# Optimization experiments

Hardware: AMD Instinct MI355X
Metric: run time of the kernel (lower is better)

Reference implementation:

```python
import jax, jax.numpy as jnp
import numpy as np

H = 8  # num_heads

def setup_inputs() -> dict:
    key = jax.random.key(0)
    ks = jax.random.split(key, 10)
    B, N, D, E = 1, 4096, 256, 65536
    s = 0.02
    return {
        "x": jax.random.normal(ks[0], (B, N, D), jnp.float32),
        "edge_index": jax.random.randint(ks[1], (2, E), 0, N, jnp.int32),
        "edge_attr": jax.random.normal(ks[2], (E, 3), jnp.float32),
        "Wq": jax.random.normal(ks[3], (D, D), jnp.float32) * s,
        "bq": jnp.zeros((D,), jnp.float32),
        "Wk": jax.random.normal(ks[4], (D, D), jnp.float32) * s,
        "bk": jnp.zeros((D,), jnp.float32),
        "Wv": jax.random.normal(ks[5], (D, D), jnp.float32) * s,
        "bv": jnp.zeros((D,), jnp.float32),
        "Wo": jax.random.normal(ks[6], (D, D), jnp.float32) * s,
        "bo": jnp.zeros((D,), jnp.float32),
        "We": jax.random.normal(ks[7], (3, H), jnp.float32) * s,
        "be": jnp.zeros((H,), jnp.float32),
    }

def reference(x, edge_index, edge_attr, Wq, bq, Wk, bk, Wv, bv, Wo, bo, We, be):
    B, N, D = x.shape
    hd = D // H
    q = (x @ Wq + bq).reshape(B, N, H, hd)
    k = (x @ Wk + bk).reshape(B, N, H, hd)
    v = (x @ Wv + bv).reshape(B, N, H, hd)
    # scores: [B, H, N, N]
    scores = jnp.einsum("bihd,bjhd->bhij", q, k) / jnp.sqrt(jnp.asarray(hd, x.dtype))
    # edge bias: torch scatter_ writes a row-constant value into column edge_tgt
    # for every query row (edge_src unused in the original). Equivalent to a
    # per-head column bias [H, N], broadcast over batch and query rows.
    eb = edge_attr @ We + be            # [E, H]
    edge_tgt = edge_index[1]
    col_bias = jnp.zeros((H, N), x.dtype).at[:, edge_tgt].set(eb.T)  # [H, N]
    scores = scores + col_bias[None, :, None, :]
    attn = jax.nn.softmax(scores, axis=-1)
    out = jnp.einsum("bhij,bjhd->bihd", attn, v).reshape(B, N, D)
    return out @ Wo + bo
```

## Files before the change

### kernel.cpp

```cpp
#include <hip/hip_runtime.h>
#include <hip/hip_bf16.h>
#include <math.h>

#define NUM_H 8
#define HD 32
#define DD 256
#define NSPLIT 2
#define KVBLK 64

typedef __attribute__((ext_vector_type(8))) short bf16x8;
typedef __attribute__((ext_vector_type(4))) float f32x4;

__device__ __forceinline__ unsigned short f2b(float f) {
  unsigned u = __builtin_bit_cast(unsigned, f);
  u += 0x7FFFu + ((u >> 16) & 1u);
  return (unsigned short)(u >> 16);
}

__device__ __forceinline__ unsigned pack2(float a, float b) {
  float2 t; t.x = a; t.y = b;
  __hip_bfloat162 r = __float22bfloat162_rn(t);
  unsigned u;
  __builtin_memcpy(&u, &r, sizeof(u));
  return u;
}

#define LOG2E 1.4426950408889634f


__global__ void sel_scatter_kernel(const int* __restrict__ tgt, int* __restrict__ sel, int E) {
  int e = blockIdx.x * 256 + threadIdx.x;
  if (e < E) atomicMax(&sel[tgt[e]], e);
}

__global__ void cvt_all(const float* __restrict__ W0, const float* __restrict__ W1,
                        const float* __restrict__ W2, const float* __restrict__ W3,
                        unsigned short* __restrict__ T0, unsigned short* __restrict__ T1,
                        unsigned short* __restrict__ T2, unsigned short* __restrict__ T3,
                        const float* __restrict__ x, unsigned short* __restrict__ xf,
                        int* __restrict__ sel, int N) {
  const int z = blockIdx.z;
  const int tid = threadIdx.x;
  if (z == 5) {
    const int b = blockIdx.x * 8 + blockIdx.y;
    if (b < (N + 255) / 256) {
      int t = b * 256 + tid;
      if (t < N) sel[t] = -1;
    }
    return;
  }
  if (z == 4) {
    const int b = blockIdx.x * 8 + blockIdx.y;
    const int ntiles = N / 16;
    for (int tt = 0; tt < ntiles / 64; ++tt) {
      const int t4 = b * (ntiles / 64) + tt;
#pragma unroll
      for (int gi = 0; gi < 2; ++gi) {
        const int g = tid + gi * 256;
        const int lr = g >> 5, kk = (g >> 2) & 7, lg = g & 3;
        const float* src = x + ((size_t)t4 * 16 + lr) * DD + kk * 32 + lg * 8;
        const float4 a = *reinterpret_cast<const float4*>(src);
        const float4 c = *reinterpret_cast<const float4*>(src + 4);
        uint4 o;
        o.x = pack2(a.x, a.y); o.y = pack2(a.z, a.w);
        o.z = pack2(c.x, c.y); o.w = pack2(c.z, c.w);
        *reinterpret_cast<uint4*>(xf + (size_t)t4 * 4096 + kk * 512 + lg * 128 + lr * 8) = o;
      }
    }
    return;
  }
  __shared__ float t[32][33];
  const float* W = (z == 0) ? W0 : (z == 1) ? W1 : (z == 2) ? W2 : W3;
  unsigned short* WF = (z == 0) ? T0 : (z == 1) ? T1 : (z == 2) ? T2 : T3;
  const int bx = blockIdx.x, by = blockIdx.y;
  const int lx = tid & 31, ly = tid >> 5;
#pragma unroll
  for (int r = 0; r < 32; r += 8)
    t[r + ly][lx] = W[(size_t)(bx * 32 + r + ly) * DD + by * 32 + lx];
  __syncthreads();
  if (tid < 128) {
    const int ct = tid & 31, lg = tid >> 5;
    bf16x8 val;
#pragma unroll
    for (int e = 0; e < 8; ++e)
      val[e] = (short)f2b(t[lg * 8 + e][ct]);
    const int off = (by * 8 + bx) * 1024 + (ct >> 4) * 512 + lg * 128 + (ct & 15) * 8;
    *reinterpret_cast<bf16x8*>(WF + off) = val;
  }
}

__global__ __launch_bounds__(256) void proj_qkv(const unsigned short* __restrict__ Xf,
                                                const unsigned short* __restrict__ WTq,
                                                const unsigned short* __restrict__ WTk,
                                                const unsigned short* __restrict__ WTv,
                                                const float* __restrict__ bq,
                                                const float* __restrict__ bk,
                                                const float* __restrict__ bv,
                                                unsigned short* __restrict__ qfrag,
                                                unsigned short* __restrict__ kfrag,
                                                unsigned short* __restrict__ vfrag,
                                                const int* __restrict__ sel,
                                                const float* __restrict__ ea,
                                                const float* __restrict__ We,
                                                const float* __restrict__ be,
                                                float* __restrict__ biasg, int N) {
  const int z = blockIdx.z;
  const int tid = threadIdx.x;
  if (z == 3) {
    const int b = blockIdx.x * 8 + blockIdx.y;
    if (b >= (N + 255) / 256) return;
    const int t = b * 256 + tid;
    if (t >= N) return;
    int e = sel[t];
    bool has = (e >= 0);
    float a0 = 0.f, a1 = 0.f, a2 = 0.f;
    if (has) {
      a0 = ea[3 * (size_t)e];
      a1 = ea[3 * (size_t)e + 1];
      a2 = ea[3 * (size_t)e + 2];
    }
#pragma unroll
    for (int h = 0; h < NUM_H; ++h) {
      float v = has ? (a0 * We[h] + a1 * We[NUM_H + h] + a2 * We[2 * NUM_H + h] + be[h]) : 0.f;
      biasg[(size_t)h * N + t] = v * LOG2E;
    }
    return;
  }
  const unsigned short* WT = (z == 0) ? WTq : (z == 1) ? WTk : WTv;
  const float* bias = (z == 0) ? bq : (z == 1) ? bk : bv;
  const int w = tid >> 6, l = tid & 63;
  const int lr = l & 15, lg = l >> 4;
  const int nt = blockIdx.x * 4 + w;
  const int n0 = nt * 16;
  const int cb = blockIdx.y;
  const int c0 = cb * 32;
  const int NT = N / 16;
  const f32x4 zero4 = {0.f, 0.f, 0.f, 0.f};
  f32x4 acc0 = zero4, acc1 = zero4;
  const unsigned short* ap = Xf + (size_t)nt * 4096 + lg * 128 + lr * 8;
  const unsigned short* bp = WT + (size_t)cb * 8192 + lg * 128 + lr * 8;
  if (z < 2) {
#pragma unroll
    for (int kk = 0; kk < 8; ++kk) {
      bf16x8 a  = *reinterpret_cast<const bf16x8*>(ap + kk * 512);
      bf16x8 b0 = *reinterpret_cast<const bf16x8*>(bp + kk * 1024);
      bf16x8 b1 = *reinterpret_cast<const bf16x8*>(bp + kk * 1024 + 512);
      acc0 = __builtin_amdgcn_mfma_f32_16x16x32_bf16(b0, a, acc0, 0, 0, 0);
      acc1 = __builtin_amdgcn_mfma_f32_16x16x32_bf16(b1, a, acc1, 0, 0, 0);
    }
    const f32x4 bv0 = *reinterpret_cast<const f32x4*>(bias + c0 + lg * 4);
    const f32x4 bv1 = *reinterpret_cast<const f32x4*>(bias + c0 + 16 + lg * 4);
    unsigned short* QK = z ? kfrag : qfrag;
    size_t base;
    int rowoff;
    if (z == 1) {
      const int j = ((nt & 3) << 4) + lr;
      const int pos = ((j >> 5) * 2 + ((j >> 2) & 1)) * 16 + (((j & 31) >> 3) << 2) + (j & 3);
      const int t16p = ((nt >> 2) << 2) + (pos >> 4);
      base = ((size_t)cb * NT + t16p) * 512;
      rowoff = (pos & 15) * 8;
    } else {
      base = ((size_t)cb * NT + nt) * 512;
      rowoff = lr * 8;
    }
    const int kf0 = (lg >> 1) * 128, ke = (lg & 1) * 4;
    uint2 o0, o1;
    o0.x = pack2(acc0[0] + bv0[0], acc0[1] + bv0[1]);
    o0.y = pack2(acc0[2] + bv0[2], acc0[3] + bv0[3]);
    o1.x = pack2(acc1[0] + bv1[0], acc1[1] + bv1[1]);
    o1.y = pack2(acc1[2] + bv1[2], acc1[3] + bv1[3]);
    *reinterpret_cast<uint2*>(QK + base + kf0 + rowoff + ke) = o0;
    *reinterpret_cast<uint2*>(QK + base + 256 + kf0 + rowoff + ke) = o1;
  } else {
#pragma unroll
    for (int kk = 0; kk < 8; ++kk) {
      bf16x8 a  = *reinterpret_cast<const bf16x8*>(ap + kk * 512);
      bf16x8 b0 = *reinterpret_cast<const bf16x8*>(bp + kk * 1024);
      bf16x8 b1 = *reinterpret_cast<const bf16x8*>(bp + kk * 1024 + 512);
      acc0 = __builtin_amdgcn_mfma_f32_16x16x32_bf16(a, b0, acc0, 0, 0, 0);
      acc1 = __builtin_amdgcn_mfma_f32_16x16x32_bf16(a, b1, acc1, 0, 0, 0);
    }
    const float bc0 = bias[c0 + lr], bc1 = bias[c0 + 16 + lr];
    const int lgf = ((n0 & 16) >> 3) + (lg >> 1);
    const int ke = (lg & 1) * 4;
    const size_t vbase = ((size_t)cb * (N / 32) + (n0 >> 5)) * 1024;
    uint2 o0, o1;
    o0.x = pack2(acc0[0] + bc0, acc0[1] + bc0);
    o0.y = pack2(acc0[2] + bc0, acc0[3] + bc0);
    o1.x = pack2(acc1[0] + bc1, acc1[1] + bc1);
    o1.y = pack2(acc1[2] + bc1, acc1[3] + bc1);
    *reinterpret_cast<uint2*>(vfrag + vbase + lgf * 128 + lr * 8 + ke) = o0;
    *reinterpret_cast<uint2*>(vfrag + vbase + 512 + lgf * 128 + lr * 8 + ke) = o1;
  }
}

__global__ __launch_bounds__(256) void proj_out(const unsigned short* __restrict__ Obf,
                                                const unsigned short* __restrict__ WT,
                                                const float* __restrict__ bias,
                                                float* __restrict__ Y, int N) {
  const int w = threadIdx.x >> 6, l = threadIdx.x & 63;
  const int lr = l & 15, lg = l >> 4;
  const int nt = blockIdx.x * 4 + w;
  const int n0 = nt * 16;
  const int cb = blockIdx.y;
  const int c0 = cb * 32;
  const f32x4 zero4 = {0.f, 0.f, 0.f, 0.f};
  f32x4 acc0 = zero4, acc1 = zero4;
  const unsigned short* ap = Obf + (size_t)nt * 4096 + lg * 128 + lr * 8;
  const unsigned short* bp = WT + (size_t)cb * 8192 + lg * 128 + lr * 8;
#pragma unroll
  for (int kk = 0; kk < 8; ++kk) {
    bf16x8 a  = *reinterpret_cast<const bf16x8*>(ap + kk * 512);
    bf16x8 b0 = *reinterpret_cast<const bf16x8*>(bp + kk * 1024);
    bf16x8 b1 = *reinterpret_cast<const bf16x8*>(bp + kk * 1024 + 512);
    acc0 = __builtin_amdgcn_mfma_f32_16x16x32_bf16(a, b0, acc0, 0, 0, 0);
    acc1 = __builtin_amdgcn_mfma_f32_16x16x32_bf16(a, b1, acc1, 0, 0, 0);
  }
  const float bc0 = bias[c0 + lr], bc1 = bias[c0 + 16 + lr];
#pragma unroll
  for (int r = 0; r < 4; ++r) {
    Y[(size_t)(n0 + lg * 4 + r) * DD + c0 + lr]      = acc0[r] + bc0;
    Y[(size_t)(n0 + lg * 4 + r) * DD + c0 + 16 + lr] = acc1[r] + bc1;
  }
}

__device__ __forceinline__ void attn_tile(const bf16x8 qf, const bf16x8* kf, const bf16x8* vf,
                                          const float* __restrict__ Bs, int tbase, int lg,
                                          float scl2, float& lsum, f32x4& oacc0, f32x4& oacc1) {
  const f32x4 zero4 = {0.f, 0.f, 0.f, 0.f};
  f32x4 sc[4];
  __builtin_amdgcn_s_setprio(1);
#pragma unroll
  for (int jf = 0; jf < 4; ++jf)
    sc[jf] = __builtin_amdgcn_mfma_f32_16x16x32_bf16(kf[jf], qf, zero4, 0, 0, 0);
  __builtin_amdgcn_s_setprio(0);

  float rsum = 0.f;
  unsigned pk[8];
#pragma unroll
  for (int jf = 0; jf < 4; ++jf) {
    const f32x4 b4 = *reinterpret_cast<const f32x4*>(
        &Bs[tbase + (jf >> 1) * 32 + lg * 8 + (jf & 1) * 4]);
    float e0 = __builtin_amdgcn_exp2f(sc[jf][0] * scl2 + b4[0]);
    float e1 = __builtin_amdgcn_exp2f(sc[jf][1] * scl2 + b4[1]);
    float e2 = __builtin_amdgcn_exp2f(sc[jf][2] * scl2 + b4[2]);
    float e3 = __builtin_amdgcn_exp2f(sc[jf][3] * scl2 + b4[3]);
    rsum += (e0 + e1) + (e2 + e3);
    pk[jf * 2]     = pack2(e0, e1);
    pk[jf * 2 + 1] = pack2(e2, e3);
  }
  rsum += __shfl_xor(rsum, 16);
  rsum += __shfl_xor(rsum, 32);
  lsum += rsum;

  bf16x8 pfA, pfB;
  __builtin_memcpy(&pfA, &pk[0], 16);
  __builtin_memcpy(&pfB, &pk[4], 16);
  __builtin_amdgcn_s_setprio(1);
  oacc0 = __builtin_amdgcn_mfma_f32_16x16x32_bf16(pfA, vf[0], oacc0, 0, 0, 0);
  oacc1 = __builtin_amdgcn_mfma_f32_16x16x32_bf16(pfA, vf[1], oacc1, 0, 0, 0);
  oacc0 = __builtin_amdgcn_mfma_f32_16x16x32_bf16(pfB, vf[2], oacc0, 0, 0, 0);
  oacc1 = __builtin_amdgcn_mfma_f32_16x16x32_bf16(pfB, vf[3], oacc1, 0, 0, 0);
  __builtin_amdgcn_s_setprio(0);
}

__global__ __launch_bounds__(256, 4) void attn_mfma(const unsigned short* __restrict__ qfrag,
                                                    const unsigned short* __restrict__ kfrag,
                                                    const unsigned short* __restrict__ vfrag,
                                                    const float* __restrict__ biasg,
                                                    float* __restrict__ Opart,
                                                    float* __restrict__ lpart, int N) {
  __shared__ float Bs[2048];
  const int tid = threadIdx.x;
  const int w = tid >> 6, l = tid & 63;
  const int lr = l & 15, lg = l >> 4;
  const int bid = blockIdx.x;
  const int h = bid & 7;
  const int rem = bid >> 3;
  const int qblk = rem & 63;
  const int s = rem >> 6;
  const int q0 = qblk * 64 + w * 16;
  const int NT = N / 16;
  const int jlo = s * (N / NSPLIT);
  const float scl2 = 0.17677669529663687f * LOG2E;

  const bf16x8 qf = *reinterpret_cast<const bf16x8*>(
      qfrag + ((size_t)h * NT + (q0 >> 4)) * 512 + l * 8);

#pragma unroll
  for (int i = 0; i < 2; ++i)
    *reinterpret_cast<float4*>(&Bs[tid * 4 + i * 1024]) =
        *reinterpret_cast<const float4*>(biasg + (size_t)h * N + jlo + tid * 4 + i * 1024);
  __syncthreads();

  const unsigned short* kb_ = kfrag + ((size_t)h * NT + (jlo >> 4)) * 512 + l * 8;
  const unsigned short* vb_ = vfrag + ((size_t)h * (N / 32) + (jlo >> 5)) * 1024 + l * 8;

  float lsum = 0.f;
  const f32x4 zero4 = {0.f, 0.f, 0.f, 0.f};
  f32x4 oacc0 = zero4, oacc1 = zero4;

#define LOADK(dst, t)                                                               \
  {                                                                                 \
    _Pragma("unroll") for (int jf = 0; jf < 4; ++jf)                                \
        dst[jf] = *reinterpret_cast<const bf16x8*>(kb_ + ((t) * 4 + jf) * 512);     \
  }
#define LOADV(dst, t)                                                               \
  {                                                                                 \
    _Pragma("unroll") for (int cd = 0; cd < 4; ++cd)                                \
        dst[cd] = *reinterpret_cast<const bf16x8*>(vb_ + ((t) * 2 + (cd >> 1)) * 1024 \
                                                   + (cd & 1) * 512);               \
  }

  const int ntiles = (N / NSPLIT) >> 6;
  bf16x8 kA[4], vA[4], kB[4], vB[4];
  LOADK(kA, 0);
  LOADV(vA, 0);
  for (int t = 0; t < ntiles; t += 2) {
    LOADK(kB, t + 1);
    LOADV(vB, t + 1);
    attn_tile(qf, kA, vA, Bs, t * 64, lg, scl2, lsum, oacc0, oacc1);
    if (t + 2 < ntiles) {
      LOADK(kA, t + 2);
      LOADV(vA, t + 2);
    }
    attn_tile(qf, kB, vB, Bs, (t + 1) * 64, lg, scl2, lsum, oacc0, oacc1);
  }
#undef LOADK
#undef LOADV

  const size_t srow = ((size_t)s * NUM_H + h) * N;
  if (lg == 0) lpart[srow + q0 + lr] = lsum;
  float* Ob = Opart + (srow + q0) * 32;
#pragma unroll
  for (int r = 0; r < 4; ++r) {
    Ob[(size_t)(lg * 4 + r) * 32 + lr]      = oacc0[r];
    Ob[(size_t)(lg * 4 + r) * 32 + 16 + lr] = oacc1[r];
  }
}

__global__ __launch_bounds__(256) void combine_kernel(const float* __restrict__ Op,
                                                      const float* __restrict__ lp,
                                                      unsigned short* __restrict__ obf, int N) {
  const int idx = blockIdx.x * 256 + threadIdx.x;
  const int d4 = idx & 7;
  const int row = idx >> 3;
  const size_t HN = (size_t)NUM_H * N;
  float wsum = 0.f;
#pragma unroll
  for (int s = 0; s < NSPLIT; ++s) wsum += lp[s * HN + row];
  const float inv = 1.f / wsum;
  float4 acc = make_float4(0.f, 0.f, 0.f, 0.f);
#pragma unroll
  for (int s = 0; s < NSPLIT; ++s) {
    const float4 v = *reinterpret_cast<const float4*>(Op + (s * HN + row) * 32 + d4 * 4);
    acc.x += v.x; acc.y += v.y; acc.z += v.z; acc.w += v.w;
  }
  const int h = row / N, n = row - h * N;
  uint2 o;
  o.x = pack2(acc.x * inv, acc.y * inv);
  o.y = pack2(acc.z * inv, acc.w * inv);
  const int off = (n >> 4) * 4096 + h * 512 + (d4 >> 1) * 128 + (n & 15) * 8 + (d4 & 1) * 4;
  *reinterpret_cast<uint2*>(obf + off) = o;
}

extern "C" void kernel_launch(void* const* d_in, const int* in_sizes, int n_in,
                              void* d_out, int out_size, void* d_ws, size_t ws_size,
                              hipStream_t stream) {
  const float* x  = (const float*)d_in[0];
  const int* eidx = (const int*)d_in[1];
  const float* ea = (const float*)d_in[2];
  const float* Wq = (const float*)d_in[3];
  const float* bq = (const float*)d_in[4];
  const float* Wk = (const float*)d_in[5];
  const float* bk = (const float*)d_in[6];
  const float* Wv = (const float*)d_in[7];
  const float* bv = (const float*)d_in[8];
  const float* Wo = (const float*)d_in[9];
  const float* bo = (const float*)d_in[10];
  const float* We = (const float*)d_in[11];
  const float* be = (const float*)d_in[12];
  float* out = (float*)d_out;

  const int N = in_sizes[0] / DD;
  const int E = in_sizes[1] / 2;
  const int* tgt = eidx + E;

  unsigned short* xf    = (unsigned short*)d_ws;
  unsigned short* qfrag = xf    + (size_t)N * DD;
  unsigned short* kfrag = qfrag + (size_t)N * DD;
  unsigned short* vfrag = kfrag + (size_t)N * DD;
  unsigned short* obf   = vfrag + (size_t)N * DD;
  unsigned short* WTq   = obf   + (size_t)N * DD;
  unsigned short* WTk = WTq + DD * DD;
  unsigned short* WTv = WTk + DD * DD;
  unsigned short* WTo = WTv + DD * DD;
  float* bias  = (float*)(WTo + DD * DD);
  float* Opart = bias + (size_t)NUM_H * N;
  float* lpart = Opart + (size_t)NSPLIT * NUM_H * N * 32;
  int*   sel   = (int*)(lpart + (size_t)NSPLIT * NUM_H * N);

  dim3 cg(8, 8, 6);
  cvt_all<<<cg, 256, 0, stream>>>(Wq, Wk, Wv, Wo, WTq, WTk, WTv, WTo, x, xf, sel, N);

  sel_scatter_kernel<<<(E + 255) / 256, 256, 0, stream>>>(tgt, sel, E);

  dim3 pg(N / 64, DD / 32, 4);
  proj_qkv<<<pg, 256, 0, stream>>>(xf, WTq, WTk, WTv, bq, bk, bv, qfrag, kfrag, vfrag,
                                   sel, ea, We, be, bias, N);

  attn_mfma<<<(N / 64) * NUM_H * NSPLIT, 256, 0, stream>>>(qfrag, kfrag, vfrag, bias,
                                                           Opart, lpart, N);

  combine_kernel<<<(NUM_H * N * 8) / 256, 256, 0, stream>>>(Opart, lpart, obf, N);

  dim3 og(N / 64, DD / 32);
  proj_out<<<og, 256, 0, stream>>>(obf, WTo, bo, out, N);
}
```

Baseline: 70.26 us.

## Process two query tiles per wave, fold scale into Q and bias into MFMA

```diff
diff --git a/kernel.cpp b/kernel.cpp
--- a/kernel.cpp
+++ b/kernel.cpp
@@ -5,8 +5,7 @@
 #define NUM_H 8
 #define HD 32
 #define DD 256
-#define NSPLIT 2
-#define KVBLK 64
+#define NSPLIT 4
 
 typedef __attribute__((ext_vector_type(8))) short bf16x8;
 typedef __attribute__((ext_vector_type(4))) float f32x4;
@@ -150,6 +149,7 @@
     }
     const f32x4 bv0 = *reinterpret_cast<const f32x4*>(bias + c0 + lg * 4);
     const f32x4 bv1 = *reinterpret_cast<const f32x4*>(bias + c0 + 16 + lg * 4);
+    const float qs = (z == 0) ? (0.17677669529663687f * LOG2E) : 1.0f;
     unsigned short* QK = z ? kfrag : qfrag;
     size_t base;
     int rowoff;
@@ -165,10 +165,10 @@
     }
     const int kf0 = (lg >> 1) * 128, ke = (lg & 1) * 4;
     uint2 o0, o1;
-    o0.x = pack2(acc0[0] + bv0[0], acc0[1] + bv0[1]);
-    o0.y = pack2(acc0[2] + bv0[2], acc0[3] + bv0[3]);
-    o1.x = pack2(acc1[0] + bv1[0], acc1[1] + bv1[1]);
-    o1.y = pack2(acc1[2] + bv1[2], acc1[3] + bv1[3]);
+    o0.x = pack2((acc0[0] + bv0[0]) * qs, (acc0[1] + bv0[1]) * qs);
+    o0.y = pack2((acc0[2] + bv0[2]) * qs, (acc0[3] + bv0[3]) * qs);
+    o1.x = pack2((acc1[0] + bv1[0]) * qs, (acc1[1] + bv1[1]) * qs);
+    o1.y = pack2((acc1[2] + bv1[2]) * qs, (acc1[3] + bv1[3]) * qs);
     *reinterpret_cast<uint2*>(QK + base + kf0 + rowoff + ke) = o0;
     *reinterpret_cast<uint2*>(QK + base + 256 + kf0 + rowoff + ke) = o1;
   } else {
@@ -224,43 +224,63 @@
   }
 }
 
-__device__ __forceinline__ void attn_tile(const bf16x8 qf, const bf16x8* kf, const bf16x8* vf,
-                                          const float* __restrict__ Bs, int tbase, int lg,
-                                          float scl2, float& lsum, f32x4& oacc0, f32x4& oacc1) {
-  const f32x4 zero4 = {0.f, 0.f, 0.f, 0.f};
-  f32x4 sc[4];
+__device__ __forceinline__ void attn_tile2(const bf16x8 qfA, const bf16x8 qfB,
+                                           const bf16x8* kf, const bf16x8* vf,
+                                           const float* __restrict__ Bs, int tbase, int lg,
+                                           float& lsA, float& lsB,
+                                           f32x4& oA0, f32x4& oA1, f32x4& oB0, f32x4& oB1) {
+  f32x4 b4[4];
+#pragma unroll
+  for (int jf = 0; jf < 4; ++jf)
+    b4[jf] = *reinterpret_cast<const f32x4*>(
+        &Bs[tbase + (jf >> 1) * 32 + lg * 8 + (jf & 1) * 4]);
+
+  f32x4 scA[4], scB[4];
   __builtin_amdgcn_s_setprio(1);
 #pragma unroll
   for (int jf = 0; jf < 4; ++jf)
-    sc[jf] = __builtin_amdgcn_mfma_f32_16x16x32_bf16(kf[jf], qf, zero4, 0, 0, 0);
+    scA[jf] = __builtin_amdgcn_mfma_f32_16x16x32_bf16(kf[jf], qfA, b4[jf], 0, 0, 0);
+#pragma unroll
+  for (int jf = 0; jf < 4; ++jf)
+    scB[jf] = __builtin_amdgcn_mfma_f32_16x16x32_bf16(kf[jf], qfB, b4[jf], 0, 0, 0);
   __builtin_amdgcn_s_setprio(0);
 
-  float rsum = 0.f;
-  unsigned pk[8];
+  unsigned pkA[8], pkB[8];
+  float rA = 0.f, rB = 0.f;
 #pragma unroll
   for (int jf = 0; jf < 4; ++jf) {
-    const f32x4 b4 = *reinterpret_cast<const f32x4*>(
-        &Bs[tbase + (jf >> 1) * 32 + lg * 8 + (jf & 1) * 4]);
-    float e0 = __builtin_amdgcn_exp2f(sc[jf][0] * scl2 + b4[0]);
-    float e1 = __builtin_amdgcn_exp2f(sc[jf][1] * scl2 + b4[1]);
-    float e2 = __builtin_amdgcn_exp2f(sc[jf][2] * scl2 + b4[2]);
-    float e3 = __builtin_amdgcn_exp2f(sc[jf][3] * scl2 + b4[3]);
-    rsum += (e0 + e1) + (e2 + e3);
-    pk[jf * 2]     = pack2(e0, e1);
-    pk[jf * 2 + 1] = pack2(e2, e3);
-  }
-  rsum += __shfl_xor(rsum, 16);
-  rsum += __shfl_xor(rsum, 32);
-  lsum += rsum;
-
-  bf16x8 pfA, pfB;
-  __builtin_memcpy(&pfA, &pk[0], 16);
-  __builtin_memcpy(&pfB, &pk[4], 16);
+    float a0 = __builtin_amdgcn_exp2f(scA[jf][0]);
+    float a1 = __builtin_amdgcn_exp2f(scA[jf][1]);
+    float a2 = __builtin_amdgcn_exp2f(scA[jf][2]);
+    float a3 = __builtin_amdgcn_exp2f(scA[jf][3]);
+    rA += (a0 + a1) + (a2 + a3);
+    pkA[jf * 2]     = pack2(a0, a1);
+    pkA[jf * 2 + 1] = pack2(a2, a3);
+    float c0 = __builtin_amdgcn_exp2f(scB[jf][0]);
+    float c1 = __builtin_amdgcn_exp2f(scB[jf][1]);
+    float c2 = __builtin_amdgcn_exp2f(scB[jf][2]);
+    float c3 = __builtin_amdgcn_exp2f(scB[jf][3]);
+    rB += (c0 + c1) + (c2 + c3);
+    pkB[jf * 2]     = pack2(c0, c1);
+    pkB[jf * 2 + 1] = pack2(c2, c3);
+  }
+  lsA += rA;
+  lsB += rB;
+
+  bf16x8 pA0, pA1, pB0, pB1;
+  __builtin_memcpy(&pA0, &pkA[0], 16);
+  __builtin_memcpy(&pA1, &pkA[4], 16);
+  __builtin_memcpy(&pB0, &pkB[0], 16);
+  __builtin_memcpy(&pB1, &pkB[4], 16);
   __builtin_amdgcn_s_setprio(1);
-  oacc0 = __builtin_amdgcn_mfma_f32_16x16x32_bf16(pfA, vf[0], oacc0, 0, 0, 0);
-  oacc1 = __builtin_amdgcn_mfma_f32_16x16x32_bf16(pfA, vf[1], oacc1, 0, 0, 0);
-  oacc0 = __builtin_amdgcn_mfma_f32_16x16x32_bf16(pfB, vf[2], oacc0, 0, 0, 0);
-  oacc1 = __builtin_amdgcn_mfma_f32_16x16x32_bf16(pfB, vf[3], oacc1, 0, 0, 0);
+  oA0 = __builtin_amdgcn_mfma_f32_16x16x32_bf16(pA0, vf[0], oA0, 0, 0, 0);
+  oA1 = __builtin_amdgcn_mfma_f32_16x16x32_bf16(pA0, vf[1], oA1, 0, 0, 0);
+  oB0 = __builtin_amdgcn_mfma_f32_16x16x32_bf16(pB0, vf[0], oB0, 0, 0, 0);
+  oB1 = __builtin_amdgcn_mfma_f32_16x16x32_bf16(pB0, vf[1], oB1, 0, 0, 0);
+  oA0 = __builtin_amdgcn_mfma_f32_16x16x32_bf16(pA1, vf[2], oA0, 0, 0, 0);
+  oA1 = __builtin_amdgcn_mfma_f32_16x16x32_bf16(pA1, vf[3], oA1, 0, 0, 0);
+  oB0 = __builtin_amdgcn_mfma_f32_16x16x32_bf16(pB1, vf[2], oB0, 0, 0, 0);
+  oB1 = __builtin_amdgcn_mfma_f32_16x16x32_bf16(pB1, vf[3], oB1, 0, 0, 0);
   __builtin_amdgcn_s_setprio(0);
 }
 
@@ -270,35 +290,34 @@
                                                     const float* __restrict__ biasg,
                                                     float* __restrict__ Opart,
                                                     float* __restrict__ lpart, int N) {
-  __shared__ float Bs[2048];
+  __shared__ float Bs[1024];
   const int tid = threadIdx.x;
   const int w = tid >> 6, l = tid & 63;
   const int lr = l & 15, lg = l >> 4;
   const int bid = blockIdx.x;
   const int h = bid & 7;
   const int rem = bid >> 3;
-  const int qblk = rem & 63;
-  const int s = rem >> 6;
-  const int q0 = qblk * 64 + w * 16;
+  const int qblk = rem & 31;
+  const int s = rem >> 5;
+  const int q0 = qblk * 128 + w * 32;
   const int NT = N / 16;
   const int jlo = s * (N / NSPLIT);
-  const float scl2 = 0.17677669529663687f * LOG2E;
-
-  const bf16x8 qf = *reinterpret_cast<const bf16x8*>(
+
+  const bf16x8 qfA = *reinterpret_cast<const bf16x8*>(
       qfrag + ((size_t)h * NT + (q0 >> 4)) * 512 + l * 8);
-
-#pragma unroll
-  for (int i = 0; i < 2; ++i)
-    *reinterpret_cast<float4*>(&Bs[tid * 4 + i * 1024]) =
-        *reinterpret_cast<const float4*>(biasg + (size_t)h * N + jlo + tid * 4 + i * 1024);
+  const bf16x8 qfB = *reinterpret_cast<const bf16x8*>(
+      qfrag + ((size_t)h * NT + (q0 >> 4) + 1) * 512 + l * 8);
+
+  *reinterpret_cast<float4*>(&Bs[tid * 4]) =
+      *reinterpret_cast<const float4*>(biasg + (size_t)h * N + jlo + tid * 4);
   __syncthreads();
 
   const unsigned short* kb_ = kfrag + ((size_t)h * NT + (jlo >> 4)) * 512 + l * 8;
   const unsigned short* vb_ = vfrag + ((size_t)h * (N / 32) + (jlo >> 5)) * 1024 + l * 8;
 
-  float lsum = 0.f;
+  float lsA = 0.f, lsB = 0.f;
   const f32x4 zero4 = {0.f, 0.f, 0.f, 0.f};
-  f32x4 oacc0 = zero4, oacc1 = zero4;
+  f32x4 oA0 = zero4, oA1 = zero4, oB0 = zero4, oB1 = zero4;
 
 #define LOADK(dst, t)                                                               \
   {                                                                                 \
@@ -319,23 +338,34 @@
   for (int t = 0; t < ntiles; t += 2) {
     LOADK(kB, t + 1);
     LOADV(vB, t + 1);
-    attn_tile(qf, kA, vA, Bs, t * 64, lg, scl2, lsum, oacc0, oacc1);
+    attn_tile2(qfA, qfB, kA, vA, Bs, t * 64, lg, lsA, lsB, oA0, oA1, oB0, oB1);
     if (t + 2 < ntiles) {
       LOADK(kA, t + 2);
       LOADV(vA, t + 2);
     }
-    attn_tile(qf, kB, vB, Bs, (t + 1) * 64, lg, scl2, lsum, oacc0, oacc1);
+    attn_tile2(qfA, qfB, kB, vB, Bs, (t + 1) * 64, lg, lsA, lsB, oA0, oA1, oB0, oB1);
   }
 #undef LOADK
 #undef LOADV
 
+  lsA += __shfl_xor(lsA, 16);
+  lsA += __shfl_xor(lsA, 32);
+  lsB += __shfl_xor(lsB, 16);
+  lsB += __shfl_xor(lsB, 32);
+
   const size_t srow = ((size_t)s * NUM_H + h) * N;
-  if (lg == 0) lpart[srow + q0 + lr] = lsum;
-  float* Ob = Opart + (srow + q0) * 32;
+  if (lg == 0) {
+    lpart[srow + q0 + lr]      = lsA;
+    lpart[srow + q0 + 16 + lr] = lsB;
+  }
+  float* ObA = Opart + (srow + q0) * 32;
+  float* ObB = Opart + (srow + q0 + 16) * 32;
 #pragma unroll
   for (int r = 0; r < 4; ++r) {
-    Ob[(size_t)(lg * 4 + r) * 32 + lr]      = oacc0[r];
-    Ob[(size_t)(lg * 4 + r) * 32 + 16 + lr] = oacc1[r];
+    ObA[(size_t)(lg * 4 + r) * 32 + lr]      = oA0[r];
+    ObA[(size_t)(lg * 4 + r) * 32 + 16 + lr] = oA1[r];
+    ObB[(size_t)(lg * 4 + r) * 32 + lr]      = oB0[r];
+    ObB[(size_t)(lg * 4 + r) * 32 + 16 + lr] = oB1[r];
   }
 }
 
@@ -409,8 +439,8 @@
   proj_qkv<<<pg, 256, 0, stream>>>(xf, WTq, WTk, WTv, bq, bk, bv, qfrag, kfrag, vfrag,
                                    sel, ea, We, be, bias, N);
 
-  attn_mfma<<<(N / 64) * NUM_H * NSPLIT, 256, 0, stream>>>(qfrag, kfrag, vfrag, bias,
-                                                           Opart, lpart, N);
+  attn_mfma<<<(N / 128) * NUM_H * NSPLIT, 256, 0, stream>>>(qfrag, kfrag, vfrag, bias,
+                                                            Opart, lpart, N);
 
   combine_kernel<<<(NUM_H * N * 8) / 256, 256, 0, stream>>>(Opart, lpart, obf, N);
 
```

After: 99.92 us. +42.2%, slower.
